# Optimization experiments

Hardware: AMD Instinct MI355X
Metric: run time of the kernel (lower is better)

## Reference

```python
import jax, jax.numpy as jnp
import numpy as np

N_NODES = 50000
N_EDGES = 800000
N_GRAPHS = 512
IN_F = 128
HEADS = 8
HEAD_C = 8
OUT_F = HEADS * HEAD_C  # 64
NEG_SLOPE = 0.2


def setup_inputs() -> dict:
    key = jax.random.key(0)
    ks = jax.random.split(key, 10)
    x = jax.random.normal(ks[0], (N_NODES, IN_F), dtype=jnp.float32)
    edge_index = jax.random.randint(ks[1], (2, N_EDGES), 0, N_NODES, dtype=jnp.int64)
    batch = jnp.sort(jax.random.randint(ks[2], (N_NODES,), 0, N_GRAPHS, dtype=jnp.int64))
    s = 0.05
    W = jax.random.normal(ks[3], (IN_F, OUT_F), dtype=jnp.float32) * s
    att_src = jax.random.normal(ks[4], (HEADS, HEAD_C), dtype=jnp.float32) * s
    att_dst = jax.random.normal(ks[5], (HEADS, HEAD_C), dtype=jnp.float32) * s
    bias = jax.random.normal(ks[6], (OUT_F,), dtype=jnp.float32) * s
    pool_w_rel = jax.random.normal(ks[7], (OUT_F, 1), dtype=jnp.float32) * s
    pool_b_rel = jax.random.normal(ks[8], (1,), dtype=jnp.float32) * s
    pool_w_root = jax.random.normal(ks[9], (OUT_F, 1), dtype=jnp.float32) * s
    return {"x": x, "edge_index": edge_index, "batch": batch, "W": W,
            "att_src": att_src, "att_dst": att_dst, "bias": bias,
            "pool_w_rel": pool_w_rel, "pool_b_rel": pool_b_rel,
            "pool_w_root": pool_w_root}


def _segment_softmax(e, seg, num_segments):
    # numerically stable scatter-softmax over segments
    m = jax.ops.segment_max(e, seg, num_segments=num_segments)
    ex = jnp.exp(e - m[seg])
    denom = jax.ops.segment_sum(ex, seg, num_segments=num_segments)
    return ex / (denom[seg] + 1e-16)


def reference(x, edge_index, batch, W, att_src, att_dst, bias,
              pool_w_rel, pool_b_rel, pool_w_root):
    N = N_NODES
    # ---- GATConv (concat heads, self-loops added, LeakyReLU 0.2) ----
    loops = jnp.arange(N, dtype=edge_index.dtype)
    src = jnp.concatenate([edge_index[0], loops])
    dst = jnp.concatenate([edge_index[1], loops])
    h = (x @ W).reshape(N, HEADS, HEAD_C)                 # [N,H,C]
    a_s = jnp.einsum('nhc,hc->nh', h, att_src)            # [N,H]
    a_d = jnp.einsum('nhc,hc->nh', h, att_dst)
    e = jax.nn.leaky_relu(a_s[src] + a_d[dst], NEG_SLOPE) # [E+N,H]
    alpha = _segment_softmax(e, dst, N)                   # softmax over incoming edges
    out = jax.ops.segment_sum(h[src] * alpha[:, :, None], dst, num_segments=N)
    out = out.reshape(N, OUT_F) + bias                    # [N,64]
    # ---- SAGPooling(min_score=-1): GraphConv score + per-graph softmax,
    #      all nodes kept (softmax scores > -1), features scaled by score ----
    s2, d2 = edge_index[0], edge_index[1]
    aggr = jax.ops.segment_sum(out[s2], d2, num_segments=N)  # add-aggregation
    score = (aggr @ pool_w_rel + pool_b_rel + out @ pool_w_root)[:, 0]  # [N]
    score = _segment_softmax(score, batch, N_GRAPHS)
    att_x = out * score[:, None]
    # ---- global_add_pool ----
    g = jax.ops.segment_sum(att_x, batch, num_segments=N_GRAPHS)  # [G,64]
    return out, g
```

## Files before the change

kernel.cpp:

```cpp
#include <hip/hip_runtime.h>

#define NN 50000
#define NE 800000
#define NG 512
#define INF_ 128
#define OUTF 64
#define CAP 64

#define NPB 98
#define BSHIFT 9
#define BNODES 512
#define BCAP 9216
#define NCHUNK 250
#define BCH 3200

#define GEMM_BLOCKS ((NN + 63) / 64)
#define FRONT_BLOCKS 1032

#define XSTRIDE 136

__device__ __forceinline__ unsigned short f2bf(float f) {
    unsigned int u = __float_as_uint(f);
    unsigned int r = (u + 0x7fffu + ((u >> 16) & 1u)) >> 16;
    return (unsigned short)r;
}
__device__ __forceinline__ float bf2f(unsigned int lo16) {
    return __uint_as_float(lo16 << 16);
}

using bf16x8 = __attribute__((ext_vector_type(8))) __bf16;
using f32x4  = __attribute__((ext_vector_type(4))) float;

__global__ __launch_bounds__(256) void k_front(
    const int* __restrict__ ei, int* __restrict__ bcnt,
    unsigned int* __restrict__ ebuf, float* __restrict__ gden,
    float* __restrict__ g_num,
    const float* __restrict__ x, const float* __restrict__ W,
    const float* __restrict__ att_src, const float* __restrict__ att_dst,
    unsigned short* __restrict__ hb, float* __restrict__ a_s,
    float* __restrict__ a_d)
{
    __shared__ union {
        struct {
            unsigned short Wt[OUTF * XSTRIDE];
            unsigned short Xs[64 * XSTRIDE];
        } g;
        struct {
            int hist[128];
            int bofs[128];
            int goff[128];
            unsigned int pk[BCH];
            unsigned int ord[BCH];
        } b;
    } sm;

    {
        int idx = blockIdx.x * 256 + threadIdx.x;
        if (idx < NG) gden[idx] = 0.f;
        else if (idx < NG + NG * OUTF) g_num[idx - NG] = 0.f;
    }

    const int t = threadIdx.x;
    int gemmIdx;
    if (blockIdx.x < 1000) {
        const int oct = blockIdx.x >> 2;
        const int r   = blockIdx.x & 3;
        if (r == 0) {
            if (t < 128) sm.b.hist[t] = 0;
            __syncthreads();

            const int e0 = oct * BCH;
            for (int i = t; i < BCH; i += 256) {
                int e = e0 + i;
                int s = ei[e];
                int d = ei[NE + e];
                int bb = d >> BSHIFT;
                unsigned int v = ((unsigned int)bb << 25) |
                                 ((unsigned int)(d & (BNODES - 1)) << 16) |
                                 (unsigned int)s;
                sm.b.pk[i] = v;
                atomicAdd(&sm.b.hist[bb], 1);
            }
            __syncthreads();

            int cntv = 0;
            if (t < 128) {
                cntv = sm.b.hist[t];
                sm.b.bofs[t] = cntv;
                sm.b.goff[t] = (t < NPB) ? atomicAdd(&bcnt[t], cntv) : 0;
            }
            __syncthreads();
            for (int off = 1; off < 128; off <<= 1) {
                int v2;
                if (t < 128) {
                    v2 = sm.b.bofs[t];
                    if (t >= off) v2 += sm.b.bofs[t - off];
                }
                __syncthreads();
                if (t < 128) sm.b.bofs[t] = v2;
                __syncthreads();
            }
            if (t < 128) {
                int excl = sm.b.bofs[t] - cntv;
                sm.b.bofs[t] = excl;
                sm.b.hist[t] = excl;
            }
            __syncthreads();

            for (int i = t; i < BCH; i += 256) {
                unsigned int v = sm.b.pk[i];
                int bb = v >> 25;
                int p = atomicAdd(&sm.b.hist[bb], 1);
                sm.b.ord[p] = v;
            }
            __syncthreads();

            for (int i = t; i < BCH; i += 256) {
                unsigned int v = sm.b.ord[i];
                int bb = v >> 25;
                int gp = sm.b.goff[bb] + (i - sm.b.bofs[bb]);
                if (gp < BCAP) ebuf[(size_t)bb * BCAP + gp] = v;
            }
            return;
        }
        gemmIdx = oct * 3 + (r - 1);
    } else {
        gemmIdx = 750 + (blockIdx.x - 1000);
    }

    const int n0 = gemmIdx * 64;

    #pragma unroll
    for (int it = 0; it < 8; it++) {
        int i = it * 256 + t;
        int k  = i >> 4;
        int n4 = (i & 15) * 4;
        float4 v = ((const float4*)W)[i];
        sm.g.Wt[(n4 + 0) * XSTRIDE + k] = f2bf(v.x);
        sm.g.Wt[(n4 + 1) * XSTRIDE + k] = f2bf(v.y);
        sm.g.Wt[(n4 + 2) * XSTRIDE + k] = f2bf(v.z);
        sm.g.Wt[(n4 + 3) * XSTRIDE + k] = f2bf(v.w);
    }

    #pragma unroll
    for (int it = 0; it < 8; it++) {
        int idx = it * 256 + t;
        int row = idx >> 5;
        int c4  = idx & 31;
        int n = n0 + row;
        if (n > NN - 1) n = NN - 1;
        float4 v = ((const float4*)(x + (size_t)n * INF_))[c4];
        ushort4 b;
        b.x = f2bf(v.x); b.y = f2bf(v.y); b.z = f2bf(v.z); b.w = f2bf(v.w);
        *(ushort4*)&sm.g.Xs[row * XSTRIDE + c4 * 4] = b;
    }
    __syncthreads();

    const int lane = t & 63;
    const int w    = t >> 6;
    const int q    = lane & 15;
    const int h4   = lane >> 4;

    f32x4 acc[4];
    #pragma unroll
    for (int ct = 0; ct < 4; ct++) acc[ct] = (f32x4){0.f, 0.f, 0.f, 0.f};

    const unsigned short* Ax = &sm.g.Xs[(w * 16 + q) * XSTRIDE + h4 * 8];
    const unsigned short* Bw = &sm.g.Wt[q * XSTRIDE + h4 * 8];

    #pragma unroll
    for (int ks = 0; ks < 4; ks++) {
        bf16x8 av = *(const bf16x8*)(Ax + ks * 32);
        #pragma unroll
        for (int ct = 0; ct < 4; ct++) {
            bf16x8 bv = *(const bf16x8*)(Bw + ct * 16 * XSTRIDE + ks * 32);
            acc[ct] = __builtin_amdgcn_mfma_f32_16x16x32_bf16(av, bv, acc[ct], 0, 0, 0);
        }
    }

    float atts[4], attd[4];
    #pragma unroll
    for (int ct = 0; ct < 4; ct++) {
        int head = 2 * ct + (q >> 3);
        atts[ct] = att_src[head * 8 + (q & 7)];
        attd[ct] = att_dst[head * 8 + (q & 7)];
    }

    #pragma unroll
    for (int r = 0; r < 4; r++) {
        const int n = n0 + w * 16 + h4 * 4 + r;
        const bool valid = (n < NN);
        if (valid) {
            #pragma unroll
            for (int ct = 0; ct < 4; ct++)
                hb[(size_t)n * OUTF + ct * 16 + q] = f2bf(acc[ct][r]);
        }
        float ps[4], pd[4];
        #pragma unroll
        for (int ct = 0; ct < 4; ct++) {
            float v = acc[ct][r];
            ps[ct] = v * atts[ct];
            pd[ct] = v * attd[ct];
        }
        #pragma unroll
        for (int m = 1; m < 8; m <<= 1) {
            #pragma unroll
            for (int ct = 0; ct < 4; ct++) {
                ps[ct] += __shfl_xor(ps[ct], m, 64);
                pd[ct] += __shfl_xor(pd[ct], m, 64);
            }
        }
        if (valid && (q & 7) == 0) {
            #pragma unroll
            for (int ct = 0; ct < 4; ct++) {
                int head = 2 * ct + (q >> 3);
                a_s[n * 8 + head] = ps[ct];
                a_d[n * 8 + head] = pd[ct];
            }
        }
    }
}

#define BHALF 256
__global__ __launch_bounds__(256) void k_build(
    const unsigned int* __restrict__ ebuf, const int* __restrict__ bcnt,
    int* __restrict__ deg, unsigned short* __restrict__ adj)
{
    __shared__ unsigned short ladj[BHALF * CAP];
    __shared__ int ldeg[BHALF];

    const int b    = blockIdx.x >> 1;
    const int half = blockIdx.x & 1;
    const int rlo  = half * BHALF;
    const int t    = threadIdx.x;

    if (t < BHALF) ldeg[t] = 0;
    __syncthreads();

    const int cnt = min(bcnt[b], BCAP);
    const unsigned int* eb = ebuf + (size_t)b * BCAP;
    for (int i = t; i < cnt; i += 256) {
        unsigned int v = eb[i];
        int drel = (v >> 16) & (BNODES - 1);
        unsigned int rr = (unsigned int)(drel - rlo);
        if (rr < BHALF) {
            int p = atomicAdd(&ldeg[rr], 1);
            if (p < CAP) ladj[rr * CAP + p] = (unsigned short)(v & 0xffffu);
        }
    }
    __syncthreads();

    const int n0 = b * BNODES + rlo;
    if (t < BHALF) {
        int n = n0 + t;
        if (n < NN) deg[n] = ldeg[t];
    }
    for (int i = t; i < BHALF * CAP / 8; i += 256) {
        int n = n0 + (i >> 3);
        if (n < NN)
            ((uint4*)(adj + (size_t)n * CAP))[i & 7] = ((const uint4*)ladj)[i];
    }
}

__global__ __launch_bounds__(256) void k_aggr(
    const unsigned short* __restrict__ hb, const float* __restrict__ a_s,
    const float* __restrict__ a_d, const int* __restrict__ deg,
    const unsigned short* __restrict__ adj, const float* __restrict__ bias,
    const float* __restrict__ w_rel, const float* __restrict__ w_root,
    float* __restrict__ out, float* __restrict__ t_rel, float* __restrict__ t_root)
{
    const int wid  = threadIdx.x >> 6;
    const int lane = threadIdx.x & 63;
    const int g    = lane >> 3;
    const int c8   = lane & 7;
    const int n    = blockIdx.x * 4 + wid;
    if (n >= NN) return;

    const float ad_n = a_d[n * 8 + c8];

    float acc[8];
    #pragma unroll
    for (int k = 0; k < 8; k++) acc[k] = 0.f;
    float den = 0.f;

    if (g == 0) {
        float e0 = a_s[n * 8 + c8] + ad_n;
        e0 = e0 > 0.f ? e0 : 0.2f * e0;
        float ex0 = __expf(e0);
        uint4 hv = *(const uint4*)(hb + (size_t)n * OUTF + c8 * 8);
        acc[0] = ex0 * bf2f(hv.x & 0xffffu); acc[1] = ex0 * bf2f(hv.x >> 16);
        acc[2] = ex0 * bf2f(hv.y & 0xffffu); acc[3] = ex0 * bf2f(hv.y >> 16);
        acc[4] = ex0 * bf2f(hv.z & 0xffffu); acc[5] = ex0 * bf2f(hv.z >> 16);
        acc[6] = ex0 * bf2f(hv.w & 0xffffu); acc[7] = ex0 * bf2f(hv.w >> 16);
        den = ex0;
    }

    const int cnt = min(deg[n], CAP);
    const unsigned short* lst = adj + (size_t)n * CAP;

    int sv[4];
    #pragma unroll
    for (int ii = 0; ii < 4; ii++) {
        int i = g + ii * 8;
        sv[ii] = (i < cnt) ? (int)lst[i] : -1;
    }
    float asl[4]; uint4 hvl[4];
    #pragma unroll
    for (int ii = 0; ii < 4; ii++) {
        int s = (sv[ii] >= 0) ? sv[ii] : n;
        asl[ii] = a_s[s * 8 + c8];
        hvl[ii] = *(const uint4*)(hb + (size_t)s * OUTF + c8 * 8);
    }
    #pragma unroll
    for (int ii = 0; ii < 4; ii++) {
        float e = asl[ii] + ad_n;
        e = e > 0.f ? e : 0.2f * e;
        float ex = (sv[ii] >= 0) ? __expf(e) : 0.f;
        uint4 hv = hvl[ii];
        acc[0] = fmaf(ex, bf2f(hv.x & 0xffffu), acc[0]);
        acc[1] = fmaf(ex, bf2f(hv.x >> 16),     acc[1]);
        acc[2] = fmaf(ex, bf2f(hv.y & 0xffffu), acc[2]);
        acc[3] = fmaf(ex, bf2f(hv.y >> 16),     acc[3]);
        acc[4] = fmaf(ex, bf2f(hv.z & 0xffffu), acc[4]);
        acc[5] = fmaf(ex, bf2f(hv.z >> 16),     acc[5]);
        acc[6] = fmaf(ex, bf2f(hv.w & 0xffffu), acc[6]);
        acc[7] = fmaf(ex, bf2f(hv.w >> 16),     acc[7]);
        den += ex;
    }
    for (int i = g + 32; i < cnt; i += 8) {
        int s = lst[i];
        float as = a_s[s * 8 + c8];
        uint4 hv = *(const uint4*)(hb + (size_t)s * OUTF + c8 * 8);
        float e = as + ad_n;
        e = e > 0.f ? e : 0.2f * e;
        float ex = __expf(e);
        acc[0] = fmaf(ex, bf2f(hv.x & 0xffffu), acc[0]);
        acc[1] = fmaf(ex, bf2f(hv.x >> 16),     acc[1]);
        acc[2] = fmaf(ex, bf2f(hv.y & 0xffffu), acc[2]);
        acc[3] = fmaf(ex, bf2f(hv.y >> 16),     acc[3]);
        acc[4] = fmaf(ex, bf2f(hv.z & 0xffffu), acc[4]);
        acc[5] = fmaf(ex, bf2f(hv.z >> 16),     acc[5]);
        acc[6] = fmaf(ex, bf2f(hv.w & 0xffffu), acc[6]);
        acc[7] = fmaf(ex, bf2f(hv.w >> 16),     acc[7]);
        den += ex;
    }

    #pragma unroll
    for (int m = 8; m < 64; m <<= 1) {
        den += __shfl_xor(den, m, 64);
        #pragma unroll
        for (int k = 0; k < 8; k++) acc[k] += __shfl_xor(acc[k], m, 64);
    }

    const float inv = 1.f / (den + 1e-16f);
    float o[8];
    #pragma unroll
    for (int k = 0; k < 8; k++) o[k] = acc[k] * inv + bias[c8 * 8 + k];

    if (g == 0) {
        float4 o0 = make_float4(o[0], o[1], o[2], o[3]);
        float4 o1 = make_float4(o[4], o[5], o[6], o[7]);
        float4* op = (float4*)(out + (size_t)n * OUTF + c8 * 8);
        op[0] = o0; op[1] = o1;
    }

    float vr = 0.f, vt = 0.f;
    #pragma unroll
    for (int k = 0; k < 8; k++) {
        vr = fmaf(o[k], w_rel[c8 * 8 + k], vr);
        vt = fmaf(o[k], w_root[c8 * 8 + k], vt);
    }
    #pragma unroll
    for (int m = 1; m < 8; m <<= 1) {
        vr += __shfl_xor(vr, m, 64);
        vt += __shfl_xor(vt, m, 64);
    }
    if (lane == 0) { t_rel[n] = vr; t_root[n] = vt; }
}

__global__ __launch_bounds__(256) void k_score_pool(
    const int* __restrict__ deg, const unsigned short* __restrict__ adj,
    const float* __restrict__ t_rel, const float* __restrict__ t_root,
    const float* __restrict__ pool_b, const int* __restrict__ batch,
    const float* __restrict__ out,
    float* __restrict__ gden, float* __restrict__ g_num)
{
    __shared__ float ex_s[32];
    __shared__ int   b_s[32];

    const int wid  = threadIdx.x >> 6;
    const int lane = threadIdx.x & 63;
    const int sub  = lane >> 3;
    const int g    = lane & 7;
    const int base_n = blockIdx.x * 32;
    const int n    = base_n + wid * 8 + sub;

    const int cnt = (n < NN) ? min(deg[n], CAP) : 0;
    const unsigned short* lst = adj + (size_t)n * CAP;
    float acc = 0.f;
    for (int i = g; i < cnt; i += 8) acc += t_rel[lst[i]];
    #pragma unroll
    for (int m = 1; m < 8; m <<= 1) acc += __shfl_xor(acc, m, 64);

    if (g == 0) {
        const int slot = wid * 8 + sub;
        if (n < NN) {
            float ex = __expf(acc + t_root[n] + pool_b[0]);
            ex_s[slot] = ex;
            b_s[slot]  = batch[n];
        } else {
            ex_s[slot] = 0.f;
            b_s[slot]  = -1;
        }
    }
    __syncthreads();

    if (threadIdx.x == 0) {
        float racc = 0.f;
        int bcur = -1;
        for (int i = 0; i < 32; i++) {
            int b = b_s[i];
            if (b != bcur) {
                if (bcur >= 0) atomicAdd(&gden[bcur], racc);
                bcur = b; racc = 0.f;
            }
            racc += ex_s[i];
        }
        if (bcur >= 0) atomicAdd(&gden[bcur], racc);
    }

    const int j = lane;
    float facc = 0.f;
    int bcur = -1;
    for (int i = 0; i < 8; i++) {
        const int slot = wid * 8 + i;
        const int n2 = base_n + slot;
        if (n2 >= NN) break;
        int b = b_s[slot];
        if (b != bcur) {
            if (bcur >= 0) atomicAdd(&g_num[bcur * OUTF + j], facc);
            bcur = b; facc = 0.f;
        }
        facc = fmaf(out[(size_t)n2 * OUTF + j], ex_s[slot], facc);
    }
    if (bcur >= 0) atomicAdd(&g_num[bcur * OUTF + j], facc);
}

__global__ __launch_bounds__(256) void k_gfinal(
    const float* __restrict__ g_num, const float* __restrict__ gden,
    float* __restrict__ g)
{
    int i = blockIdx.x * 256 + threadIdx.x;
    if (i < NG * OUTF) g[i] = g_num[i] / (gden[i >> 6] + 1e-16f);
}

extern "C" void kernel_launch(void* const* d_in, const int* in_sizes, int n_in,
                              void* d_out, int out_size, void* d_ws, size_t ws_size,
                              hipStream_t stream)
{
    const float* x        = (const float*)d_in[0];
    const int*   ei       = (const int*)  d_in[1];
    const int*   batch    = (const int*)  d_in[2];
    const float* W        = (const float*)d_in[3];
    const float* att_src  = (const float*)d_in[4];
    const float* att_dst  = (const float*)d_in[5];
    const float* bias     = (const float*)d_in[6];
    const float* w_rel    = (const float*)d_in[7];
    const float* pool_b   = (const float*)d_in[8];
    const float* w_root   = (const float*)d_in[9];

    float* out_nodes = (float*)d_out;
    float* g_out     = (float*)d_out + (size_t)NN * OUTF;

    char* base = (char*)d_ws;
    unsigned short* hb = (unsigned short*)(base);
    float* a_s       = (float*)(base +  6400000);
    float* a_d       = (float*)(base +  8000000);
    float* t_rel     = (float*)(base +  9600000);
    float* t_root    = (float*)(base +  9800000);
    float* gden      = (float*)(base + 10000000);
    float* g_num     = (float*)(base + 10002048);
    int*   deg       = (int*)  (base + 10133120);
    unsigned short* adjl = (unsigned short*)(base + 10333120);
    unsigned int* ebuf = (unsigned int*)(base + 16733120);
    int*   bcnt      = (int*)  (base + 20345792);

    hipMemsetAsync(bcnt, 0, 512, stream);

    k_front<<<FRONT_BLOCKS, 256, 0, stream>>>(
        ei, bcnt, ebuf, gden, g_num,
        x, W, att_src, att_dst, hb, a_s, a_d);
    k_build<<<NPB * 2, 256, 0, stream>>>(ebuf, bcnt, deg, adjl);
    k_aggr<<<(NN + 3) / 4, 256, 0, stream>>>(hb, a_s, a_d, deg, adjl, bias,
                                             w_rel, w_root, out_nodes, t_rel, t_root);
    k_score_pool<<<(NN + 31) / 32, 256, 0, stream>>>(deg, adjl, t_rel, t_root,
                                                     pool_b, batch, out_nodes,
                                                     gden, g_num);
    k_gfinal<<<(NG * OUTF + 255) / 256, 256, 0, stream>>>(g_num, gden, g_out);
}
```

Measured before the change: 162.0 us.

## Compute pooling scores from bucketed edge buffer with shared-memory atomics

```diff
diff --git a/kernel.cpp b/kernel.cpp
--- a/kernel.cpp
+++ b/kernel.cpp
@@ -378,70 +378,86 @@
     if (lane == 0) { t_rel[n] = vr; t_root[n] = vt; }
 }
 
-__global__ __launch_bounds__(256) void k_score_pool(
-    const int* __restrict__ deg, const unsigned short* __restrict__ adj,
+#define POOL_T 512
+__global__ __launch_bounds__(POOL_T) void k_pool(
+    const unsigned int* __restrict__ ebuf, const int* __restrict__ bcnt,
     const float* __restrict__ t_rel, const float* __restrict__ t_root,
     const float* __restrict__ pool_b, const int* __restrict__ batch,
     const float* __restrict__ out,
     float* __restrict__ gden, float* __restrict__ g_num)
 {
-    __shared__ float ex_s[32];
-    __shared__ int   b_s[32];
-
-    const int wid  = threadIdx.x >> 6;
-    const int lane = threadIdx.x & 63;
-    const int sub  = lane >> 3;
-    const int g    = lane & 7;
-    const int base_n = blockIdx.x * 32;
-    const int n    = base_n + wid * 8 + sub;
-
-    const int cnt = (n < NN) ? min(deg[n], CAP) : 0;
-    const unsigned short* lst = adj + (size_t)n * CAP;
-    float acc = 0.f;
-    for (int i = g; i < cnt; i += 8) acc += t_rel[lst[i]];
-    #pragma unroll
-    for (int m = 1; m < 8; m <<= 1) acc += __shfl_xor(acc, m, 64);
-
-    if (g == 0) {
-        const int slot = wid * 8 + sub;
-        if (n < NN) {
-            float ex = __expf(acc + t_root[n] + pool_b[0]);
-            ex_s[slot] = ex;
-            b_s[slot]  = batch[n];
-        } else {
-            ex_s[slot] = 0.f;
-            b_s[slot]  = -1;
-        }
-    }
+    __shared__ float sc[BNODES];
+    __shared__ int   bat[BNODES];
+
+    const int b = blockIdx.x;
+    const int t = threadIdx.x;
+    for (int i = t; i < BNODES; i += POOL_T) sc[i] = 0.f;
     __syncthreads();
 
-    if (threadIdx.x == 0) {
-        float racc = 0.f;
-        int bcur = -1;
-        for (int i = 0; i < 32; i++) {
-            int b = b_s[i];
-            if (b != bcur) {
-                if (bcur >= 0) atomicAdd(&gden[bcur], racc);
-                bcur = b; racc = 0.f;
-            }
-            racc += ex_s[i];
-        }
-        if (bcur >= 0) atomicAdd(&gden[bcur], racc);
-    }
-
-    const int j = lane;
+    const int cnt = min(bcnt[b], BCAP);
+    const unsigned int* eb = ebuf + (size_t)b * BCAP;
+    int i = t;
+    for (; i + 3 * POOL_T < cnt; i += 4 * POOL_T) {
+        unsigned int v0 = eb[i];
+        unsigned int v1 = eb[i + POOL_T];
+        unsigned int v2 = eb[i + 2 * POOL_T];
+        unsigned int v3 = eb[i + 3 * POOL_T];
+        float r0 = t_rel[v0 & 0xffffu];
+        float r1 = t_rel[v1 & 0xffffu];
+        float r2 = t_rel[v2 & 0xffffu];
+        float r3 = t_rel[v3 & 0xffffu];
+        atomicAdd(&sc[(v0 >> 16) & (BNODES - 1)], r0);
+        atomicAdd(&sc[(v1 >> 16) & (BNODES - 1)], r1);
+        atomicAdd(&sc[(v2 >> 16) & (BNODES - 1)], r2);
+        atomicAdd(&sc[(v3 >> 16) & (BNODES - 1)], r3);
+    }
+    for (; i < cnt; i += POOL_T) {
+        unsigned int v = eb[i];
+        atomicAdd(&sc[(v >> 16) & (BNODES - 1)], t_rel[v & 0xffffu]);
+    }
+    __syncthreads();
+
+    const int n0 = b * BNODES;
+    const int n  = n0 + t;
+    const float pb = pool_b[0];
+    float ex = 0.f;
+    int bb = -1;
+    if (n < NN) {
+        ex = __expf(sc[t] + t_root[n] + pb);
+        bb = batch[n];
+    }
+    {
+        const int lane = t & 63;
+        float v = ex;
+        #pragma unroll
+        for (int m = 1; m < 64; m <<= 1) {
+            float ov = __shfl_up(v, m, 64);
+            int   ob = __shfl_up(bb, m, 64);
+            if (lane >= m && ob == bb) v += ov;
+        }
+        int bnext = __shfl_down(bb, 1, 64);
+        if (bb >= 0 && (lane == 63 || bnext != bb))
+            atomicAdd(&gden[bb], v);
+    }
+    sc[t]  = ex;
+    bat[t] = bb;
+    __syncthreads();
+
+    const int wv = t >> 6;
+    const int j  = t & 63;
+    const int i0 = wv * 64;
     float facc = 0.f;
     int bcur = -1;
-    for (int i = 0; i < 8; i++) {
-        const int slot = wid * 8 + i;
-        const int n2 = base_n + slot;
+    for (int k = 0; k < 64; k++) {
+        const int ii = i0 + k;
+        const int n2 = n0 + ii;
         if (n2 >= NN) break;
-        int b = b_s[slot];
-        if (b != bcur) {
+        int bk = bat[ii];
+        if (bk != bcur) {
             if (bcur >= 0) atomicAdd(&g_num[bcur * OUTF + j], facc);
-            bcur = b; facc = 0.f;
-        }
-        facc = fmaf(out[(size_t)n2 * OUTF + j], ex_s[slot], facc);
+            bcur = bk; facc = 0.f;
+        }
+        facc = fmaf(out[(size_t)n2 * OUTF + j], sc[ii], facc);
     }
     if (bcur >= 0) atomicAdd(&g_num[bcur * OUTF + j], facc);
 }
@@ -493,8 +509,8 @@
     k_build<<<NPB * 2, 256, 0, stream>>>(ebuf, bcnt, deg, adjl);
     k_aggr<<<(NN + 3) / 4, 256, 0, stream>>>(hb, a_s, a_d, deg, adjl, bias,
                                              w_rel, w_root, out_nodes, t_rel, t_root);
-    k_score_pool<<<(NN + 31) / 32, 256, 0, stream>>>(deg, adjl, t_rel, t_root,
-                                                     pool_b, batch, out_nodes,
-                                                     gden, g_num);
+    k_pool<<<NPB, POOL_T, 0, stream>>>(ebuf, bcnt, t_rel, t_root,
+                                       pool_b, batch, out_nodes,
+                                       gden, g_num);
     k_gfinal<<<(NG * OUTF + 255) / 256, 256, 0, stream>>>(g_num, gden, g_out);
 }
```

After: 181.4 us. 12.0% more time.
